# Kernel tuning notes

Hardware: AMD Instinct MI355X
Metric: run time of the kernel (lower is better)

## Reference

```python
import jax, jax.numpy as jnp
import numpy as np

BS, N, F, G, H, L, HFC, C, E = 8, 15135, 64, 73, 256, 3, 512, 2, 242160

def setup_inputs() -> dict:
    key = jax.random.key(0)
    ks = jax.random.split(key, 16)
    s = 0.02
    return {
        "x": jax.random.normal(ks[0], (BS, N, F), jnp.float32),
        "batch": jnp.zeros((BS,), jnp.int64),
        "edge_index": jax.random.randint(ks[1], (2, E), 0, N, jnp.int64),
        "nodes_graphlets": jax.random.uniform(ks[2], (N, G), jnp.float32),
        "W1": jax.random.normal(ks[3], (F + G, H), jnp.float32) * s,
        "b1": jnp.zeros((H,), jnp.float32),
        "W2": jax.random.normal(ks[4], (H, H), jnp.float32) * s,
        "b2": jnp.zeros((H,), jnp.float32),
        "W3": jax.random.normal(ks[5], (H, H), jnp.float32) * s,
        "b3": jnp.zeros((H,), jnp.float32),
        "fc_W": jax.random.normal(ks[6], (L * H, 1), jnp.float32) * s,
        "fc_b": jnp.zeros((1,), jnp.float32),
        "lin1_W": jax.random.normal(ks[7], (N, HFC), jnp.float32) * s,
        "lin1_b": jnp.zeros((HFC,), jnp.float32),
        "lin2_W": jax.random.normal(ks[8], (HFC, C), jnp.float32) * s,
        "lin2_b": jnp.zeros((C,), jnp.float32),
    }


def reference(x, batch, edge_index, nodes_graphlets, W1, b1, W2, b2, W3, b3,
              fc_W, fc_b, lin1_W, lin1_b, lin2_W, lin2_b):
    bs, n, _ = x.shape
    row, col = edge_index[0], edge_index[1]
    # GCN normalization with self-loops (edge_weight = 1): D^-1/2 (A+I) D^-1/2
    deg = jnp.zeros((n,), x.dtype).at[col].add(1.0) + 1.0
    dis = jax.lax.rsqrt(deg)
    norm = dis[row] * dis[col]          # [E]
    deg_inv = 1.0 / deg                 # self-loop coefficient dis[i]^2

    def gcn_conv(h, W, b):
        hw = h @ W                                  # [bs, n, H]
        msg = hw[:, row, :] * norm[None, :, None]   # gather src, scale
        agg = jnp.zeros_like(hw).at[:, col, :].add(msg)
        agg = agg + hw * deg_inv[None, :, None]     # self loops
        return agg + b

    # graphlet_mode == 'input': concat graphlet features to node features
    pe = jnp.broadcast_to(nodes_graphlets[None], (bs,) + nodes_graphlets.shape)
    h = jnp.concatenate([x, pe], axis=2)            # [bs, n, F+G]

    h1 = jax.nn.elu(gcn_conv(h, W1, b1))
    h2 = jax.nn.elu(gcn_conv(h1, W2, b2))
    h3 = jax.nn.elu(gcn_conv(h2, W3, b3))

    # mode == 'cat': stack along new last dim then flatten (torch stack+view order)
    hc = jnp.stack([h1, h2, h3], axis=-1).reshape(bs, n, -1)  # [bs, n, H*L]
    g = (hc @ fc_W + fc_b).reshape(bs, n)                     # [bs, n_genes]

    z = jax.nn.elu(g @ lin1_W + lin1_b)   # dropout: eval mode -> identity
    out = z @ lin2_W + lin2_b
    return jax.nn.log_softmax(out, axis=-1)
```

## Files before the change

### kernel.cpp

```cpp
#include <hip/hip_runtime.h>
#include <hip/hip_bf16.h>

using bf16 = __hip_bfloat16;
typedef short s16x8 __attribute__((ext_vector_type(8)));
typedef short s16x4 __attribute__((ext_vector_type(4)));
typedef float f32x4 __attribute__((ext_vector_type(4)));
typedef float f32x2 __attribute__((ext_vector_type(2)));

#define BSZ   8
#define NN    15135
#define FF    64
#define GG    73
#define HH    256
#define EE    242160
#define K1P   160
#define MREAL (BSZ * NN)
#define MPAD  (946 * 128)
#define HFC   512
#define NCHUNK 64
#define NCHUNKS ((NN + NCHUNK - 1) / NCHUNK)
#define SCANB  ((NN + 255) / 256)
#define FP8_INV_SCALE 0.015625f

#define GLOAD_LDS16(gp, lp)                                                     \
    __builtin_amdgcn_global_load_lds(                                           \
        (const __attribute__((address_space(1))) void*)(gp),                    \
        (__attribute__((address_space(3))) void*)(lp), 16, 0, 0)

__device__ __forceinline__ int colmap(int p) {
    return (p & 192) | ((p & 3) << 4) | ((p >> 2) & 15);
}

__global__ void k_deg(const int* __restrict__ col, int* __restrict__ cnt, int e) {
    int i = blockIdx.x * blockDim.x + threadIdx.x;
    if (i < e) atomicAdd(&cnt[col[i]], 1);
}

__global__ __launch_bounds__(256)
void k_scanA(const int* __restrict__ cnt, int* __restrict__ cursor,
             int* __restrict__ bsum) {
    __shared__ int ws[4];
    int i = blockIdx.x * 256 + threadIdx.x;
    int tid = threadIdx.x, lane = tid & 63, wid = tid >> 6;
    int v = (i < NN) ? cnt[i] : 0;
    int s = v;
    #pragma unroll
    for (int off = 1; off < 64; off <<= 1) {
        int t = __shfl_up(s, off);
        if (lane >= off) s += t;
    }
    if (lane == 63) ws[wid] = s;
    __syncthreads();
    int pre = 0;
    #pragma unroll
    for (int w = 0; w < 4; ++w) pre += (w < wid) ? ws[w] : 0;
    int incl = pre + s;
    if (i < NN) cursor[i] = incl;
    if (tid == 255) bsum[blockIdx.x] = incl;
}

__global__ __launch_bounds__(64)
void k_scanB(int* __restrict__ bsum, int* __restrict__ offs) {
    int t = threadIdx.x;
    int v = (t < SCANB) ? bsum[t] : 0;
    int s = v;
    #pragma unroll
    for (int off = 1; off < 64; off <<= 1) {
        int x = __shfl_up(s, off);
        if (t >= off) s += x;
    }
    if (t < SCANB) bsum[t] = s - v;
    if (t == 63) offs[NN] = s;
}

__global__ __launch_bounds__(256)
void k_scanC(const int* __restrict__ cnt, int* __restrict__ cursor,
             const int* __restrict__ bsum, int* __restrict__ offs,
             float* __restrict__ dis, float* __restrict__ dinv) {
    int i = blockIdx.x * 256 + threadIdx.x;
    if (i >= NN) return;
    int v = cnt[i];
    int excl = cursor[i] - v + bsum[blockIdx.x];
    offs[i] = excl;
    cursor[i] = excl;
    float d = (float)(v + 1);
    dis[i]  = rsqrtf(d);
    dinv[i] = (1.0f / d) * FP8_INV_SCALE;
}

__global__ void k_csr(const int* __restrict__ row, const int* __restrict__ col,
                      int* __restrict__ cursor, const float* __restrict__ dis,
                      int2* __restrict__ cpack, int e) {
    int i = blockIdx.x * blockDim.x + threadIdx.x;
    if (i >= e) return;
    int r = row[i], c = col[i];
    int p = atomicAdd(&cursor[c], 1);
    cpack[p] = make_int2(r, __float_as_int(dis[r] * dis[c] * FP8_INV_SCALE));
}

__global__ void k_prep_h0(const float* __restrict__ x, const float* __restrict__ gl,
                          bf16* __restrict__ h0) {
    int idx = blockIdx.x * blockDim.x + threadIdx.x;
    if (idx >= MREAL * (K1P / 8)) return;
    int m = idx / (K1P / 8);
    int q = idx - m * (K1P / 8);
    int j0 = q * 8;
    int n = m % NN;
    s16x8 o;
    #pragma unroll
    for (int k = 0; k < 8; ++k) {
        int j = j0 + k;
        float val;
        if (j < FF) val = x[(size_t)m * FF + j];
        else if (j < FF + GG) val = gl[(size_t)n * GG + (j - FF)];
        else val = 0.f;
        o[k] = (short)__bfloat16_as_ushort(__float2bfloat16(val));
    }
    *(s16x8*)&h0[(size_t)m * K1P + j0] = o;
}

__global__ void k_prep_w(const float* __restrict__ W, bf16* __restrict__ WT,
                         int K, int Kpad, int perm) {
    int idx = blockIdx.x * blockDim.x + threadIdx.x;
    if (idx >= 256 * Kpad) return;
    int nn = idx / Kpad, kk = idx - nn * Kpad;
    int ks = perm ? colmap(kk) : kk;
    WT[idx] = __float2bfloat16(kk < K ? W[(size_t)ks * 256 + nn] : 0.f);
}

#define BK 32
template <int K>
__global__ __launch_bounds__(256)
void k_gemm(const bf16* __restrict__ A, const bf16* __restrict__ BT,
            unsigned char* __restrict__ C) {
    __shared__ __align__(16) short As[128 * BK];
    __shared__ __align__(16) short Bs[128 * BK];
    const int tid  = threadIdx.x;
    const int bm   = blockIdx.x * 128;
    const int bn   = blockIdx.y * 128;
    const int lane = tid & 63, wave = tid >> 6;
    const int wm   = (wave >> 1) * 64, wn = (wave & 1) * 64;
    const int fr   = lane & 15, quad = lane >> 4;
    const int r    = tid >> 2;
    const int c    = (tid & 3) * 8;

    const bf16* Ap0 = A  + (size_t)(bm + r) * K + c;
    const bf16* Ap1 = Ap0 + (size_t)64 * K;
    const bf16* Bp0 = BT + (size_t)(bn + r) * K + c;
    const bf16* Bp1 = Bp0 + (size_t)64 * K;
    short* AsT0 = As + tid * 8;
    short* AsT1 = As + 2048 + tid * 8;
    short* BsT0 = Bs + tid * 8;
    short* BsT1 = Bs + 2048 + tid * 8;

    f32x4 acc[4][4] = {};

    for (int k0 = 0; k0 < K; k0 += BK) {
        GLOAD_LDS16(Ap0 + k0, AsT0);
        GLOAD_LDS16(Ap1 + k0, AsT1);
        GLOAD_LDS16(Bp0 + k0, BsT0);
        GLOAD_LDS16(Bp1 + k0, BsT1);
        __syncthreads();
        s16x8 af[4], bfv[4];
        #pragma unroll
        for (int i = 0; i < 4; ++i)
            af[i] = *(const s16x8*)&As[(wm + i * 16 + fr) * BK + quad * 8];
        #pragma unroll
        for (int j = 0; j < 4; ++j)
            bfv[j] = *(const s16x8*)&Bs[(wn + j * 16 + fr) * BK + quad * 8];
        #pragma unroll
        for (int i = 0; i < 4; ++i)
            #pragma unroll
            for (int j = 0; j < 4; ++j)
                acc[i][j] = __builtin_amdgcn_mfma_f32_16x16x32_bf16(
                    af[i], bfv[j], acc[i][j], 0, 0, 0);
        __syncthreads();
    }

    #pragma unroll
    for (int i = 0; i < 4; ++i) {
        int rbase = bm + wm + i * 16 + quad * 4;
        #pragma unroll
        for (int rr = 0; rr < 4; ++rr) {
            int row = rbase + rr;
            if (row >= MREAL) continue;
            unsigned wpack = (unsigned)__builtin_amdgcn_cvt_pk_fp8_f32(
                acc[i][0][rr] * 64.f, acc[i][1][rr] * 64.f, 0, false);
            wpack = (unsigned)__builtin_amdgcn_cvt_pk_fp8_f32(
                acc[i][2][rr] * 64.f, acc[i][3][rr] * 64.f, (int)wpack, true);
            *(unsigned*)&C[(size_t)row * 256 + bn + wn + fr * 4] = wpack;
        }
    }
}

#define AGG_GRP 512
#define AGG_STRIDE (AGG_GRP * 4)
__global__ __launch_bounds__(256)
void k_agg(const unsigned char* __restrict__ hw, bf16* __restrict__ hout,
           const int* __restrict__ offs, const int2* __restrict__ cpack,
           const float* __restrict__ dinv,
           const float* __restrict__ bias, const float* __restrict__ fcW,
           float* __restrict__ g, int writeH) {
    const int b    = blockIdx.x & 7;
    const int grp  = blockIdx.x >> 3;
    const int wid  = threadIdx.x >> 6;
    const int lane = threadIdx.x & 63;
    const int wv   = grp * 4 + wid;
    const unsigned c4 = lane * 4;

    const unsigned char* hwb = hw + (size_t)b * NN * 256;

    float bias4[4], fw4[4];
    #pragma unroll
    for (int k = 0; k < 4; ++k) {
        int cl = colmap((int)c4 + k);
        bias4[k] = bias[cl];
        fw4[k]   = fcW[3 * cl];
    }

    for (int v0 = wv; v0 < NN; v0 += AGG_STRIDE) {
        const int v   = __builtin_amdgcn_readfirstlane(v0);
        const int beg = __builtin_amdgcn_readfirstlane(offs[v]);
        const int end = __builtin_amdgcn_readfirstlane(offs[v + 1]);
        const float di = dinv[v];
        f32x2 a01, a23;
        {
            unsigned q = *(const unsigned*)(hwb + (((unsigned)v) << 8) + c4);
            f32x2 t0 = __builtin_amdgcn_cvt_pk_f32_fp8(q, false);
            f32x2 t1 = __builtin_amdgcn_cvt_pk_f32_fp8(q, true);
            f32x2 dd = {di, di};
            a01 = dd * t0;
            a23 = dd * t1;
        }

        #define EDGE1(qv, mv) {                                            \
            f32x2 t0 = __builtin_amdgcn_cvt_pk_f32_fp8((qv), false);       \
            f32x2 t1 = __builtin_amdgcn_cvt_pk_f32_fp8((qv), true);        \
            f32x2 mm = {(mv), (mv)};                                       \
            a01 += mm * t0;                                                \
            a23 += mm * t1; }

        int e = beg;
        while (e + 8 <= end) {
            int2 ep[8];
            #pragma unroll
            for (int u = 0; u < 8; ++u) ep[u] = cpack[e + u];
            unsigned q[8];
            #pragma unroll
            for (int u = 0; u < 8; ++u)
                q[u] = *(const unsigned*)(hwb + (((unsigned)ep[u].x) << 8) + c4);
            #pragma unroll
            for (int u = 0; u < 8; ++u) EDGE1(q[u], __int_as_float(ep[u].y));
            e += 8;
        }
        if (e + 4 <= end) {
            int2 ep[4];
            #pragma unroll
            for (int u = 0; u < 4; ++u) ep[u] = cpack[e + u];
            unsigned q[4];
            #pragma unroll
            for (int u = 0; u < 4; ++u)
                q[u] = *(const unsigned*)(hwb + (((unsigned)ep[u].x) << 8) + c4);
            #pragma unroll
            for (int u = 0; u < 4; ++u) EDGE1(q[u], __int_as_float(ep[u].y));
            e += 4;
        }
        if (e + 2 <= end) {
            int2 ep0 = cpack[e], ep1 = cpack[e + 1];
            unsigned q0 = *(const unsigned*)(hwb + (((unsigned)ep0.x) << 8) + c4);
            unsigned q1 = *(const unsigned*)(hwb + (((unsigned)ep1.x) << 8) + c4);
            EDGE1(q0, __int_as_float(ep0.y));
            EDGE1(q1, __int_as_float(ep1.y));
            e += 2;
        }
        if (e < end) {
            int2 ep0 = cpack[e];
            unsigned q0 = *(const unsigned*)(hwb + (((unsigned)ep0.x) << 8) + c4);
            EDGE1(q0, __int_as_float(ep0.y));
        }
        #undef EDGE1

        float acc4[4] = {a01[0], a01[1], a23[0], a23[1]};
        float p = 0.f;
        s16x4 o4;
        #pragma unroll
        for (int k = 0; k < 4; ++k) {
            float hv = acc4[k] + bias4[k];
            hv = hv > 0.f ? hv : (__expf(hv) - 1.0f);
            o4[k] = (short)__bfloat16_as_ushort(__float2bfloat16(hv));
            p += hv * fw4[k];
        }
        if (writeH)
            *(s16x4*)&hout[((size_t)b * NN + v) * 256 + c4] = o4;

        #pragma unroll
        for (int off = 32; off; off >>= 1) p += __shfl_xor(p, off);
        if (lane == 0) g[(size_t)b * NN + v] += p;
    }
}

__global__ __launch_bounds__(256)
void k_lin1(const float* __restrict__ g, const float* __restrict__ fcb,
            const float* __restrict__ W, float* __restrict__ zpart) {
    const int ny = blockIdx.x;
    const int n0 = ny * NCHUNK;
    const int cnt = min(NCHUNK, NN - n0);
    const int tid = threadIdx.x;
    __shared__ float sg[8][NCHUNK];
    float fb = fcb[0];
    for (int idx = tid; idx < 8 * NCHUNK; idx += 256) {
        int b = idx / NCHUNK, nn = idx - b * NCHUNK;
        sg[b][nn] = (nn < cnt) ? (g[(size_t)b * NN + n0 + nn] + fb) : 0.f;
    }
    __syncthreads();
    float2 acc[8] = {};
    for (int nn = 0; nn < cnt; ++nn) {
        float2 w = *(const float2*)&W[(size_t)(n0 + nn) * HFC + tid * 2];
        #pragma unroll
        for (int b = 0; b < 8; ++b) {
            float gv = sg[b][nn];
            acc[b].x += gv * w.x;
            acc[b].y += gv * w.y;
        }
    }
    #pragma unroll
    for (int b = 0; b < 8; ++b)
        *(float2*)&zpart[(size_t)ny * 4096 + b * 512 + tid * 2] = acc[b];
}

__global__ __launch_bounds__(256)
void k_lin1red(const float* __restrict__ zpart, float* __restrict__ zacc) {
    int t = blockIdx.x * 256 + threadIdx.x;
    float s = 0.f;
    for (int c = 0; c < NCHUNKS; ++c) s += zpart[(size_t)c * 4096 + t];
    zacc[t] = s;
}

__global__ __launch_bounds__(512)
void k_final(const float* __restrict__ zacc, const float* __restrict__ l1b,
             const float* __restrict__ W2, const float* __restrict__ l2b,
             float* __restrict__ out) {
    __shared__ float r0[512], r1[512];
    int t = threadIdx.x;
    for (int b = 0; b < 8; ++b) {
        float zv = zacc[b * HFC + t] + l1b[t];
        zv = zv > 0.f ? zv : (__expf(zv) - 1.0f);
        r0[t] = zv * W2[t * 2 + 0];
        r1[t] = zv * W2[t * 2 + 1];
        __syncthreads();
        for (int s = 256; s; s >>= 1) {
            if (t < s) { r0[t] += r0[t + s]; r1[t] += r1[t + s]; }
            __syncthreads();
        }
        if (t == 0) {
            float o0 = r0[0] + l2b[0], o1 = r1[0] + l2b[1];
            float m = fmaxf(o0, o1);
            float lse = m + logf(expf(o0 - m) + expf(o1 - m));
            out[b * 2 + 0] = o0 - lse;
            out[b * 2 + 1] = o1 - lse;
        }
        __syncthreads();
    }
}

extern "C" void kernel_launch(void* const* d_in, const int* in_sizes, int n_in,
                              void* d_out, int out_size, void* d_ws, size_t ws_size,
                              hipStream_t stream) {
    const float* x    = (const float*)d_in[0];
    const int*   eidx = (const int*)d_in[2];
    const float* gl   = (const float*)d_in[3];
    const float* W1   = (const float*)d_in[4];
    const float* b1   = (const float*)d_in[5];
    const float* W2   = (const float*)d_in[6];
    const float* b2   = (const float*)d_in[7];
    const float* W3   = (const float*)d_in[8];
    const float* b3   = (const float*)d_in[9];
    const float* fcW  = (const float*)d_in[10];
    const float* fcb  = (const float*)d_in[11];
    const float* l1W  = (const float*)d_in[12];
    const float* l1b  = (const float*)d_in[13];
    const float* l2W  = (const float*)d_in[14];
    const float* l2b  = (const float*)d_in[15];
    float* out = (float*)d_out;

    size_t off = 0;
    auto alloc = [&](size_t bytes) {
        void* p = (char*)d_ws + off;
        off += (bytes + 255) & ~(size_t)255;
        return p;
    };
    bf16* bufA          = (bf16*)alloc((size_t)MPAD * 256 * 2);
    unsigned char* bufC = (unsigned char*)alloc((size_t)MPAD * 256);
    bf16* W1T      = (bf16*)alloc(256 * K1P * 2);
    bf16* W2T      = (bf16*)alloc(256 * 256 * 2);
    bf16* W3T      = (bf16*)alloc(256 * 256 * 2);
    int*  deg_cnt  = (int*)alloc(NN * 4);
    int*  offs     = (int*)alloc((NN + 1) * 4);
    int*  cursor   = (int*)alloc(NN * 4);
    int*  bsum     = (int*)alloc(SCANB * 4);
    float* dis     = (float*)alloc(NN * 4);
    float* dinv    = (float*)alloc(NN * 4);
    int2* cpack    = (int2*)alloc((size_t)EE * 8);
    float* g       = (float*)alloc((size_t)BSZ * NN * 4);

    float* zpart = (float*)bufC;
    float* zacc  = (float*)(bufC + (8 << 20));

    hipMemsetAsync(deg_cnt, 0, NN * 4, stream);
    hipMemsetAsync(g, 0, (size_t)BSZ * NN * 4, stream);

    const int* erow = eidx;
    const int* ecol = eidx + EE;

    k_deg<<<(EE + 255) / 256, 256, 0, stream>>>(ecol, deg_cnt, EE);
    k_scanA<<<SCANB, 256, 0, stream>>>(deg_cnt, cursor, bsum);
    k_scanB<<<1, 64, 0, stream>>>(bsum, offs);
    k_scanC<<<SCANB, 256, 0, stream>>>(deg_cnt, cursor, bsum, offs, dis, dinv);
    k_csr<<<(EE + 255) / 256, 256, 0, stream>>>(erow, ecol, cursor, dis,
                                                cpack, EE);

    k_prep_h0<<<(MREAL * (K1P / 8) + 255) / 256, 256, 0, stream>>>(x, gl, bufA);
    k_prep_w<<<(256 * K1P + 255) / 256, 256, 0, stream>>>(W1, W1T, FF + GG, K1P, 0);
    k_prep_w<<<(256 * 256 + 255) / 256, 256, 0, stream>>>(W2, W2T, 256, 256, 1);
    k_prep_w<<<(256 * 256 + 255) / 256, 256, 0, stream>>>(W3, W3T, 256, 256, 1);

    dim3 ggrid(MPAD / 128, 2);
    dim3 agrid(8 * AGG_GRP);

    k_gemm<K1P><<<ggrid, 256, 0, stream>>>(bufA, W1T, bufC);
    k_agg<<<agrid, 256, 0, stream>>>(bufC, bufA, offs, cpack, dinv,
                                     b1, fcW + 0, g, 1);
    k_gemm<256><<<ggrid, 256, 0, stream>>>(bufA, W2T, bufC);
    k_agg<<<agrid, 256, 0, stream>>>(bufC, bufA, offs, cpack, dinv,
                                     b2, fcW + 1, g, 1);
    k_gemm<256><<<ggrid, 256, 0, stream>>>(bufA, W3T, bufC);
    k_agg<<<agrid, 256, 0, stream>>>(bufC, bufA, offs, cpack, dinv,
                                     b3, fcW + 2, g, 0);

    k_lin1<<<NCHUNKS, 256, 0, stream>>>(g, fcb, l1W, zpart);
    k_lin1red<<<16, 256, 0, stream>>>(zpart, zacc);
    k_final<<<1, 512, 0, stream>>>(zacc, l1b, l2W, l2b, out);
}
```

Measured before the change: 465.9 us.

## Retile GEMM to 64x256 blocks, fold FP8 scale into weights, merge weight prep

The GEMM now uses 64-row by full-256-column tiles, so each A row tile is loaded once instead of twice across two column blocks. Each wave owns a 64-column slab. The x64 FP8 output scale moves from the epilogue into the bf16 weights during prep. The three weight-prep launches are merged into one kernel to cut launch overhead. Possible costs are less A-fragment reuse per wave, more B traffic per block, and a scaling change that could slightly alter bf16 rounding.

```diff
diff --git a/kernel.cpp b/kernel.cpp
--- a/kernel.cpp
+++ b/kernel.cpp
@@ -119,13 +119,23 @@
     *(s16x8*)&h0[(size_t)m * K1P + j0] = o;
 }
 
-__global__ void k_prep_w(const float* __restrict__ W, bf16* __restrict__ WT,
-                         int K, int Kpad, int perm) {
+__global__ void k_prep_w3(const float* __restrict__ W1, const float* __restrict__ W2,
+                          const float* __restrict__ W3, bf16* __restrict__ W1T,
+                          bf16* __restrict__ W2T, bf16* __restrict__ W3T) {
     int idx = blockIdx.x * blockDim.x + threadIdx.x;
-    if (idx >= 256 * Kpad) return;
-    int nn = idx / Kpad, kk = idx - nn * Kpad;
-    int ks = perm ? colmap(kk) : kk;
-    WT[idx] = __float2bfloat16(kk < K ? W[(size_t)ks * 256 + nn] : 0.f);
+    if (idx < 256 * K1P) {
+        int nn = idx / K1P, kk = idx - nn * K1P;
+        W1T[idx] = __float2bfloat16(
+            kk < FF + GG ? 64.f * W1[(size_t)kk * 256 + nn] : 0.f);
+    } else if (idx < 256 * K1P + 65536) {
+        int j = idx - 256 * K1P;
+        int nn = j >> 8, kk = j & 255;
+        W2T[j] = __float2bfloat16(64.f * W2[(size_t)colmap(kk) * 256 + nn]);
+    } else if (idx < 256 * K1P + 2 * 65536) {
+        int j = idx - 256 * K1P - 65536;
+        int nn = j >> 8, kk = j & 255;
+        W3T[j] = __float2bfloat16(64.f * W3[(size_t)colmap(kk) * 256 + nn]);
+    }
 }
 
 #define BK 32
@@ -133,38 +143,33 @@
 __global__ __launch_bounds__(256)
 void k_gemm(const bf16* __restrict__ A, const bf16* __restrict__ BT,
             unsigned char* __restrict__ C) {
-    __shared__ __align__(16) short As[128 * BK];
-    __shared__ __align__(16) short Bs[128 * BK];
+    __shared__ __align__(16) short As[64 * BK];
+    __shared__ __align__(16) short Bs[256 * BK];
     const int tid  = threadIdx.x;
-    const int bm   = blockIdx.x * 128;
-    const int bn   = blockIdx.y * 128;
+    const int bm   = blockIdx.x * 64;
     const int lane = tid & 63, wave = tid >> 6;
-    const int wm   = (wave >> 1) * 64, wn = (wave & 1) * 64;
+    const int wn   = wave * 64;
     const int fr   = lane & 15, quad = lane >> 4;
     const int r    = tid >> 2;
     const int c    = (tid & 3) * 8;
 
-    const bf16* Ap0 = A  + (size_t)(bm + r) * K + c;
-    const bf16* Ap1 = Ap0 + (size_t)64 * K;
-    const bf16* Bp0 = BT + (size_t)(bn + r) * K + c;
-    const bf16* Bp1 = Bp0 + (size_t)64 * K;
-    short* AsT0 = As + tid * 8;
-    short* AsT1 = As + 2048 + tid * 8;
-    short* BsT0 = Bs + tid * 8;
-    short* BsT1 = Bs + 2048 + tid * 8;
+    const bf16* Ap = A  + (size_t)(bm + r) * K + c;
+    const bf16* Bp = BT + (size_t)r * K + c;
+    short* AsT = As + tid * 8;
+    short* BsT = Bs + tid * 8;
 
     f32x4 acc[4][4] = {};
 
     for (int k0 = 0; k0 < K; k0 += BK) {
-        GLOAD_LDS16(Ap0 + k0, AsT0);
-        GLOAD_LDS16(Ap1 + k0, AsT1);
-        GLOAD_LDS16(Bp0 + k0, BsT0);
-        GLOAD_LDS16(Bp1 + k0, BsT1);
+        GLOAD_LDS16(Ap + k0, AsT);
+        #pragma unroll
+        for (int q = 0; q < 4; ++q)
+            GLOAD_LDS16(Bp + (size_t)(q * 64) * K + k0, BsT + q * 64 * BK);
         __syncthreads();
         s16x8 af[4], bfv[4];
         #pragma unroll
         for (int i = 0; i < 4; ++i)
-            af[i] = *(const s16x8*)&As[(wm + i * 16 + fr) * BK + quad * 8];
+            af[i] = *(const s16x8*)&As[(i * 16 + fr) * BK + quad * 8];
         #pragma unroll
         for (int j = 0; j < 4; ++j)
             bfv[j] = *(const s16x8*)&Bs[(wn + j * 16 + fr) * BK + quad * 8];
@@ -179,16 +184,16 @@
 
     #pragma unroll
     for (int i = 0; i < 4; ++i) {
-        int rbase = bm + wm + i * 16 + quad * 4;
+        int rbase = bm + i * 16 + quad * 4;
         #pragma unroll
         for (int rr = 0; rr < 4; ++rr) {
             int row = rbase + rr;
             if (row >= MREAL) continue;
             unsigned wpack = (unsigned)__builtin_amdgcn_cvt_pk_fp8_f32(
-                acc[i][0][rr] * 64.f, acc[i][1][rr] * 64.f, 0, false);
+                acc[i][0][rr], acc[i][1][rr], 0, false);
             wpack = (unsigned)__builtin_amdgcn_cvt_pk_fp8_f32(
-                acc[i][2][rr] * 64.f, acc[i][3][rr] * 64.f, (int)wpack, true);
-            *(unsigned*)&C[(size_t)row * 256 + bn + wn + fr * 4] = wpack;
+                acc[i][2][rr], acc[i][3][rr], (int)wpack, true);
+            *(unsigned*)&C[(size_t)row * 256 + wn + fr * 4] = wpack;
         }
     }
 }
@@ -420,11 +425,10 @@
                                                 cpack, EE);
 
     k_prep_h0<<<(MREAL * (K1P / 8) + 255) / 256, 256, 0, stream>>>(x, gl, bufA);
-    k_prep_w<<<(256 * K1P + 255) / 256, 256, 0, stream>>>(W1, W1T, FF + GG, K1P, 0);
-    k_prep_w<<<(256 * 256 + 255) / 256, 256, 0, stream>>>(W2, W2T, 256, 256, 1);
-    k_prep_w<<<(256 * 256 + 255) / 256, 256, 0, stream>>>(W3, W3T, 256, 256, 1);
-
-    dim3 ggrid(MPAD / 128, 2);
+    k_prep_w3<<<(256 * K1P + 2 * 65536 + 255) / 256, 256, 0, stream>>>(
+        W1, W2, W3, W1T, W2T, W3T);
+
+    dim3 ggrid(MPAD / 64);
     dim3 agrid(8 * AGG_GRP);
 
     k_gemm<K1P><<<ggrid, 256, 0, stream>>>(bufA, W1T, bufC);
```

Result: no change. 459.8 us (-1.3%).
